# Kernel tuning notes

Hardware: AMD Instinct MI355X
Metric: run time of the kernel (lower is better)

## Reference

```python
import jax, jax.numpy as jnp
import numpy as np
import math

H_IMG, W_IMG = 800, 1216
STRIDES = [4, 8, 16, 32, 64]
SIZES = [32, 64, 128, 256, 512]
RATIOS = [0.5, 1.0, 2.0]
NUM_PER_LEVEL = [(-(-H_IMG // s)) * (-(-W_IMG // s)) * len(RATIOS) for s in STRIDES]
A_TOTAL = sum(NUM_PER_LEVEL)  # 728973
B = 4
PRE_NMS = 1000   # pre_nms_top_n['testing']
POST_NMS = 1000  # post_nms_top_n['testing']
NMS_TH = 0.7
MIN_SIZE = 1e-3
BBOX_XFORM_CLIP = math.log(1000.0 / 16)
NEG = -1e10
LEVELS_NP = np.repeat(np.arange(len(NUM_PER_LEVEL)), NUM_PER_LEVEL).astype(np.int32)


def _make_anchors():
    out = []
    for stride, size in zip(STRIDES, SIZES):
        fh, fw = -(-H_IMG // stride), -(-W_IMG // stride)
        r = np.sqrt(np.asarray(RATIOS, dtype=np.float64))
        ws, hs = size / r, size * r
        base = np.stack([-ws / 2, -hs / 2, ws / 2, hs / 2], axis=1)  # [3,4]
        sx = np.arange(fw, dtype=np.float64) * stride
        sy = np.arange(fh, dtype=np.float64) * stride
        gy, gx = np.meshgrid(sy, sx, indexing='ij')
        shifts = np.stack([gx.ravel(), gy.ravel(), gx.ravel(), gy.ravel()], axis=1)
        out.append((shifts[:, None, :] + base[None]).reshape(-1, 4))
    return np.concatenate(out, 0).astype(np.float32)


def setup_inputs() -> dict:
    key = jax.random.key(0)
    k1, k2 = jax.random.split(key)
    objectness = jax.random.normal(k1, (B, A_TOTAL), dtype=jnp.float32)
    deltas = jax.random.normal(k2, (B, A_TOTAL, 4), dtype=jnp.float32) * 0.2
    anchors = jnp.asarray(_make_anchors())
    return {'objectness': objectness, 'deltas': deltas, 'anchors': anchors}


def _decode(deltas, anchors):
    # BoxCoder.decode with weights (1,1,1,1)
    wa = anchors[:, 2] - anchors[:, 0]
    ha = anchors[:, 3] - anchors[:, 1]
    cxa = anchors[:, 0] + 0.5 * wa
    cya = anchors[:, 1] + 0.5 * ha
    dx, dy = deltas[..., 0], deltas[..., 1]
    dw = jnp.minimum(deltas[..., 2], BBOX_XFORM_CLIP)
    dh = jnp.minimum(deltas[..., 3], BBOX_XFORM_CLIP)
    cx = dx * wa + cxa
    cy = dy * ha + cya
    w = jnp.exp(dw) * wa
    h = jnp.exp(dh) * ha
    return jnp.stack([cx - 0.5 * w, cy - 0.5 * h, cx + 0.5 * w, cy + 0.5 * h], axis=-1)


def _topk_per_level(obj):
    # _get_top_n_idx: independent top-k within each anchor level, indices offset
    idxs, off = [], 0
    for n in NUM_PER_LEVEL:
        k = min(PRE_NMS, n)
        _, ti = jax.lax.top_k(obj[:, off:off + n], k)
        idxs.append(ti + off)
        off += n
    return jnp.concatenate(idxs, axis=1)


def _pairwise_iou(b):
    area = (b[:, 2] - b[:, 0]) * (b[:, 3] - b[:, 1])
    lt = jnp.maximum(b[:, None, :2], b[None, :, :2])
    rb = jnp.minimum(b[:, None, 2:], b[None, :, 2:])
    wh = jnp.clip(rb - lt, 0.0)
    inter = wh[..., 0] * wh[..., 1]
    return inter / (area[:, None] + area[None, :] - inter)


def _filter_image(boxes, scores, lvl):
    # clip_boxes_to_image
    x1 = jnp.clip(boxes[:, 0], 0.0, W_IMG)
    y1 = jnp.clip(boxes[:, 1], 0.0, H_IMG)
    x2 = jnp.clip(boxes[:, 2], 0.0, W_IMG)
    y2 = jnp.clip(boxes[:, 3], 0.0, H_IMG)
    boxes = jnp.stack([x1, y1, x2, y2], axis=1)
    # remove_small_boxes (as a validity mask; fixed shapes under jit)
    valid = ((x2 - x1) >= MIN_SIZE) & ((y2 - y1) >= MIN_SIZE)
    scores = jnp.where(valid, scores, NEG)
    N = boxes.shape[0]
    # batched_nms: offset boxes per level so levels never overlap
    sg_boxes = jax.lax.stop_gradient(boxes)
    offset = lvl.astype(boxes.dtype) * (sg_boxes.max() + 1.0)
    order = jnp.argsort(-jax.lax.stop_gradient(scores))
    iou = _pairwise_iou(sg_boxes[order] + offset[order][:, None])  # [N,N]
    idx = jnp.arange(N)
    def body(i, keep):
        sup = (iou[i] > NMS_TH) & keep[i] & (idx > i)
        return keep & ~sup
    keep = jax.lax.fori_loop(0, N, body, valid[order])
    # kept entries in score order, then truncate to POST_NMS (fixed shape)
    prio = jnp.where(keep, idx, N)
    sel = jnp.argsort(prio)[:POST_NMS]
    kept = keep[sel]
    src = order[sel]
    out_b = jnp.where(kept[:, None], boxes[src], 0.0)
    out_s = jnp.where(kept, scores[src], NEG)
    return out_b, out_s


def reference(objectness, deltas, anchors):
    proposals = _decode(deltas, anchors)                      # [B,A,4]
    top_idx = _topk_per_level(objectness)                     # [B,5000]
    obj_sel = jnp.take_along_axis(objectness, top_idx, axis=1)
    prop_sel = jnp.take_along_axis(proposals, top_idx[..., None], axis=1)
    lvl_sel = jnp.asarray(LEVELS_NP)[top_idx]
    boxes, scores = jax.vmap(_filter_image)(prop_sel, obj_sel, lvl_sel)
    return boxes, scores  # [B,POST_NMS,4], [B,POST_NMS]
```

## Files before the change

### kernel.cpp

```cpp
#include <hip/hip_runtime.h>
#include <stdint.h>

#pragma clang fp contract(off)

#define B_IMGS   4
#define NLVL     5
#define A_TOTAL  242991
#define NSEL     4741
#define NBUCK    8192
#define BSHIFT   19
#define CAND_CAP 2048
#define POST_NMS 1000
#define NBL      (B_IMGS * NLVL)
#define NMS_TH   0.7f
#define NEGV     (-1e10f)
#define W_IMGF   1216.0f
#define H_IMGF   800.0f
#define MIN_SZ   1e-3f
#define BBOX_CLIP 4.135166556742356f

#define NSLICE_PER_IMG 34

__device__ __forceinline__ int lvl_k(int l) { return (l == 4) ? 741 : 1000; }

__device__ __forceinline__ unsigned flipf(float f) {
    unsigned u = __float_as_uint(f);
    return u ^ (unsigned)(((int)u >> 31) | 0x80000000);
}
__device__ __forceinline__ float unflipf(unsigned os) {
    unsigned u = (os & 0x80000000u) ? (os ^ 0x80000000u) : ~os;
    return __uint_as_float(u);
}

__device__ __forceinline__ void async_cp16(const void* g, void* l) {
    __builtin_amdgcn_global_load_lds(
        (const __attribute__((address_space(1))) unsigned*)g,
        (__attribute__((address_space(3))) unsigned*)l,
        16, 0, 0);
}

static constexpr size_t OFF_BM5   = 0;
static constexpr size_t OFF_CNT   = 128;
static constexpr size_t OFF_DI    = 208;
static constexpr size_t OFF_D2    = 224;
static constexpr size_t OFF_HSL   = 256;
static constexpr size_t OFF_PSL   = OFF_HSL  + (size_t)B_IMGS * NSLICE_PER_IMG * NBUCK * 4;
static constexpr size_t OFF_CAND  = OFF_PSL  + (size_t)B_IMGS * NSLICE_PER_IMG * 256 * 4;
static constexpr size_t OFF_SEL   = OFF_CAND + (size_t)NBL * CAND_CAP * 8;
static constexpr size_t OFF_BOXR  = OFF_SEL  + (size_t)B_IMGS * NSEL * 8;
static constexpr size_t OFF_SCR   = OFF_BOXR + (size_t)B_IMGS * NSEL * 16;
static constexpr size_t OFF_BOXL  = OFF_SCR  + (size_t)B_IMGS * NSEL * 4;
static constexpr size_t OFF_VAL   = OFF_BOXL + (size_t)B_IMGS * NSEL * 16;
static constexpr size_t OFF_RMAP  = OFF_VAL  + (size_t)B_IMGS * NSEL * 4;
static constexpr size_t OFF_KEEP  = OFF_RMAP + (size_t)B_IMGS * NSEL * 4;
static constexpr size_t OFF_MASK  = (OFF_KEEP + (size_t)B_IMGS * NSEL * 4 + 15) & ~(size_t)15;
static constexpr size_t WS_NEED   = OFF_MASK + (size_t)NBL * 1024 * 16 * 8;

#define HBLK_PER_IMG 34
__global__ __launch_bounds__(512) void k_hist(const float* __restrict__ obj,
                                              unsigned* __restrict__ hist_sl,
                                              unsigned* __restrict__ part_sl,
                                              unsigned* __restrict__ cntz) {
    __shared__ __align__(16) unsigned lh[NBUCK];
    const int tid = threadIdx.x;
    const int b = blockIdx.x / HBLK_PER_IMG;
    const int r = blockIdx.x - b * HBLK_PER_IMG;
    if (r == 33) {
        if (b == 0 && tid < 28) cntz[tid] = 0;
        return;
    }
    int sofs, sub, chunk, lstart, n;
    if (r < 24)      { sofs = 0;  sub = r;      chunk = 7600; lstart = 0;      n = 182400; }
    else if (r < 30) { sofs = 24; sub = r - 24; chunk = 7600; lstart = 182400; n = 45600; }
    else if (r < 32) { sofs = 30; sub = r - 30; chunk = 5700; lstart = 228000; n = 11400; }
    else             { sofs = 32; sub = 0;      chunk = 2850; lstart = 239400; n = 2850; }
    #pragma unroll
    for (int i = tid; i < NBUCK; i += 512) lh[i] = 0;
    __syncthreads();
    const int s0 = sub * chunk;
    const int m = min(chunk, n - s0);
    const float* src = obj + (size_t)b * A_TOTAL + lstart + s0;
    const int peel0 = (int)(((16u - ((unsigned)(uintptr_t)src & 15u)) & 15u) >> 2);
    const int peel  = (peel0 < m) ? peel0 : m;
    const int nv    = (m - peel) >> 2;
    const float4* s4 = (const float4*)(src + peel);
    const int tail0 = peel + (nv << 2);
#define H1(f) atomicAdd(&lh[flipf(f) >> BSHIFT], 1u)
#define H4(v) do { H1((v).x); H1((v).y); H1((v).z); H1((v).w); } while (0)
    if (tid < peel) H1(src[tid]);
    for (int i = tid; i < nv; i += 2048) {
        if (i + 1536 < nv) {
            float4 a0 = s4[i], a1 = s4[i + 512], a2 = s4[i + 1024], a3 = s4[i + 1536];
            H4(a0); H4(a1); H4(a2); H4(a3);
        } else {
            float4 a0 = s4[i]; H4(a0);
            if (i + 512  < nv) { float4 a = s4[i + 512];  H4(a); }
            if (i + 1024 < nv) { float4 a = s4[i + 1024]; H4(a); }
        }
    }
    for (int i = tail0 + tid; i < m; i += 512) H1(src[i]);
#undef H4
#undef H1
    __syncthreads();
    const int slice = b * NSLICE_PER_IMG + sofs + sub;
    unsigned* gh = hist_sl + (size_t)slice * NBUCK;
    #pragma unroll
    for (int i = tid; i < NBUCK / 4; i += 512)
        ((uint4*)gh)[i] = ((const uint4*)lh)[i];
    if (tid < 256) {
        unsigned s = 0;
        #pragma unroll
        for (int i = 0; i < 32; ++i) s += lh[tid * 32 + ((i + tid) & 31)];
        part_sl[(size_t)slice * 256 + tid] = s;
    }
}

#define CBLK_PER_IMG 65
__global__ __launch_bounds__(256) void k_compact(const float* __restrict__ obj,
                                                 const unsigned* __restrict__ hist_sl,
                                                 const unsigned* __restrict__ part_sl,
                                                 unsigned* __restrict__ cnt,
                                                 unsigned long long* __restrict__ cand) {
    __shared__ unsigned long long sbuf[CAND_CAP];
    __shared__ unsigned wsum[4];
    __shared__ unsigned fcnt[4];
    __shared__ unsigned s_cum, s_thr, lcnt, gbase;
    const int tid = threadIdx.x;
    const int b = blockIdx.x / CBLK_PER_IMG;
    const int r = blockIdx.x - b * CBLK_PER_IMG;
    int l, sofs, nsub, sub, chunk, lstart, n;
    if (r < 48)      { l = 0; sofs = 0;  nsub = 24; sub = r;      chunk = 3800; lstart = 0;      n = 182400; }
    else if (r < 60) { l = 1; sofs = 24; nsub = 6;  sub = r - 48; chunk = 3800; lstart = 182400; n = 45600; }
    else if (r < 63) { l = 2; sofs = 30; nsub = 2;  sub = r - 60; chunk = 3800; lstart = 228000; n = 11400; }
    else if (r == 63){ l = 3; sofs = 32; nsub = 1;  sub = 0;      chunk = 2850; lstart = 239400; n = 2850; }
    else             { l = 4; sofs = 33; nsub = 0;  sub = 0;      chunk = 741;  lstart = 242250; n = 741; }
    const int bl = b * NLVL + l;
    const int kl = lvl_k(l);
    if (tid == 0) { lcnt = 0; s_cum = 0; }
    __syncthreads();
    unsigned T = 0;
    if (l < 4) {
        const int lane = tid & 63, wv = tid >> 6;
        const unsigned* pb = part_sl + (size_t)(b * NSLICE_PER_IMG + sofs) * 256 + (255 - tid);
        unsigned x = 0;
        #pragma unroll 6
        for (int s = 0; s < nsub; ++s) x += pb[(size_t)s * 256];
        #pragma unroll
        for (int d = 1; d < 64; d <<= 1) {
            unsigned up = __shfl_up(x, d);
            if (lane >= d) x += up;
        }
        if (lane == 63) wsum[wv] = x;
        __syncthreads();
        unsigned add = 0;
        #pragma unroll
        for (int u = 0; u < 3; ++u) if (u < wv) add += wsum[u];
        const unsigned suffix = x + add;
        unsigned long long bm = __ballot(suffix >= (unsigned)kl);
        if (lane == 0) fcnt[wv] = (unsigned)__popcll(bm);
        __syncthreads();
        const int chnk = (int)(fcnt[0] + fcnt[1] + fcnt[2] + fcnt[3]) - 1;
        if ((255 - tid) == chnk + 1) s_cum = suffix;
        __syncthreads();
        if (tid < 64) {
            unsigned y = 0;
            if (tid < 32) {
                const unsigned* hb = hist_sl + (size_t)(b * NSLICE_PER_IMG + sofs) * NBUCK
                                   + chnk * 32 + (31 - tid);
                #pragma unroll 6
                for (int s = 0; s < nsub; ++s) y += hb[(size_t)s * NBUCK];
            }
            #pragma unroll
            for (int d = 1; d < 32; d <<= 1) {
                unsigned up = __shfl_up(y, d);
                if (tid >= d) y += up;
            }
            unsigned suf2 = s_cum + y;
            unsigned long long bm2 = __ballot((tid < 32) && (suf2 >= (unsigned)kl));
            if (tid == 0) {
                int istar = (int)__popcll(bm2) - 1;
                s_thr = (unsigned)(chnk * 32 + istar);
            }
        }
        __syncthreads();
        T = s_thr;
    }
    const int s0 = sub * chunk;
    const int m = min(chunk, n - s0);
    const int abase = lstart + s0;
    const float* src = obj + (size_t)b * A_TOTAL + abase;
    const int peel0 = (int)(((16u - ((unsigned)(uintptr_t)src & 15u)) & 15u) >> 2);
    const int peel  = (peel0 < m) ? peel0 : m;
    const int nv    = (m - peel) >> 2;
    const float4* s4 = (const float4*)(src + peel);
    const int tail0 = peel + (nv << 2);
#define E1(f, idx) do { unsigned os_ = flipf(f); \
    if ((os_ >> BSHIFT) >= T) { \
        unsigned slot = atomicAdd(&lcnt, 1u); \
        if (slot < CAND_CAP) \
            sbuf[slot] = (((unsigned long long)(~os_)) << 32) | (unsigned)(idx); \
    } } while (0)
#define E4(v, gb) do { E1((v).x, (gb)); E1((v).y, (gb) + 1); \
                       E1((v).z, (gb) + 2); E1((v).w, (gb) + 3); } while (0)
    if (tid < peel) E1(src[tid], abase + tid);
    for (int i = tid; i < nv; i += 512) {
        const int gb0 = abase + peel + (i << 2);
        if (i + 256 < nv) {
            float4 a0 = s4[i], a1 = s4[i + 256];
            E4(a0, gb0);
            E4(a1, gb0 + 1024);
        } else {
            float4 a0 = s4[i];
            E4(a0, gb0);
        }
    }
    for (int i = tail0 + tid; i < m; i += 256) E1(src[i], abase + i);
#undef E4
#undef E1
    __syncthreads();
    unsigned total = lcnt; if (total > CAND_CAP) total = CAND_CAP;
    if (tid == 0) gbase = atomicAdd(&cnt[bl], total);
    __syncthreads();
    const unsigned gb = gbase;
    for (unsigned i = tid; i < total; i += 256) {
        unsigned g = gb + i;
        if (g < CAND_CAP)
            cand[(size_t)bl * CAND_CAP + g] = sbuf[i];
    }
}

__device__ __forceinline__ int lbound_lds(const unsigned long long* s, int len,
                                          unsigned long long key) {
    int lo = 0, hi = len;
    while (lo < hi) {
        int mid = (lo + hi) >> 1;
        if (s[mid] < key) lo = mid + 1; else hi = mid;
    }
    return lo;
}

__global__ __launch_bounds__(1024) void k_sortdec(
        const unsigned long long* __restrict__ cand, const unsigned* __restrict__ cnt,
        unsigned long long* __restrict__ sel,
        const float* __restrict__ deltas, const float* __restrict__ anchors,
        float* __restrict__ boxes_r, float* __restrict__ score_r,
        float* __restrict__ boxes_l, int* __restrict__ valid_l,
        int* __restrict__ rankmap, unsigned* __restrict__ boxmax5,
        unsigned* __restrict__ bar_i) {
    __shared__ __align__(16) char smem[38016];
    __shared__ float wmax[16];
    const int bl = blockIdx.x;
    const int b = bl / NLVL, l = bl - (bl / NLVL) * NLVL;
    const int tid = threadIdx.x;

    {
        unsigned long long* keys = (unsigned long long*)smem;
        int m = (int)cnt[bl];
        if (m > CAND_CAP) m = CAND_CAP;
        for (int i = tid; i < CAND_CAP; i += 1024)
            keys[i] = (i < m) ? cand[(size_t)bl * CAND_CAP + i] : ~0ULL;
        __syncthreads();
        for (int k = 2; k <= CAND_CAP; k <<= 1) {
            for (int j = k >> 1; j > 0; j >>= 1) {
                int i = ((tid / j) * (j << 1)) + (tid % j);
                int p = i + j;
                bool up = ((i & k) == 0);
                unsigned long long a = keys[i], c = keys[p];
                if ((a > c) == up) { keys[i] = c; keys[p] = a; }
                __syncthreads();
            }
        }
        int kl = lvl_k(l);
        for (int q = tid; q < kl; q += 1024)
            sel[(size_t)b * NSEL + l * 1000 + q] = keys[q];
    }
    __syncthreads();

    if (tid == 0) {
        __threadfence();
        __hip_atomic_fetch_add(bar_i + b, 1u, __ATOMIC_RELAXED, __HIP_MEMORY_SCOPE_AGENT);
        while (__hip_atomic_load(bar_i + b, __ATOMIC_RELAXED, __HIP_MEMORY_SCOPE_AGENT)
               < (unsigned)NLVL)
            __builtin_amdgcn_s_sleep(2);
        __threadfence();
    }
    __syncthreads();

    unsigned long long* skey = (unsigned long long*)smem;
    for (int i = tid; i < NSEL; i += 1024)
        skey[i] = sel[(size_t)b * NSEL + i];
    __syncthreads();
    const int sub = l;
    int p = sub * 1024 + tid;
    bool on = p < NSEL;
    float mx = 0.0f;
    if (on) {
        int l2i = p / 1000;
        int q = p - l2i * 1000;
        unsigned long long key = skey[p];
        unsigned a = (unsigned)(key & 0xFFFFFFFFu);
        unsigned os = ~((unsigned)(key >> 32));
        if (a >= A_TOTAL) a = 0;
        float score = unflipf(os);
        int r = q;
        for (int l2 = 0; l2 < NLVL; ++l2) {
            if (l2 == l2i) continue;
            r += lbound_lds(skey + l2 * 1000, lvl_k(l2), key);
        }
        const float* dv = deltas + ((size_t)b * A_TOTAL + a) * 4;
        const float* av = anchors + (size_t)a * 4;
        float ax1 = av[0], ay1 = av[1], ax2 = av[2], ay2 = av[3];
        float wa = ax2 - ax1, ha = ay2 - ay1;
        float cxa = ax1 + 0.5f * wa, cya = ay1 + 0.5f * ha;
        float dx = dv[0], dy = dv[1];
        float dw = fminf(dv[2], BBOX_CLIP), dh = fminf(dv[3], BBOX_CLIP);
        float cx = dx * wa + cxa, cy = dy * ha + cya;
        float w = expf(dw) * wa, h = expf(dh) * ha;
        float x1 = cx - 0.5f * w, y1 = cy - 0.5f * h;
        float x2 = cx + 0.5f * w, y2 = cy + 0.5f * h;
        float x1c = fminf(fmaxf(x1, 0.0f), W_IMGF);
        float y1c = fminf(fmaxf(y1, 0.0f), H_IMGF);
        float x2c = fminf(fmaxf(x2, 0.0f), W_IMGF);
        float y2c = fminf(fmaxf(y2, 0.0f), H_IMGF);
        int valid = ((x2c - x1c) >= MIN_SZ) && ((y2c - y1c) >= MIN_SZ);
        mx = fmaxf(fmaxf(x1c, y1c), fmaxf(x2c, y2c));
        size_t rp = (size_t)b * NSEL + r;
        boxes_r[rp * 4 + 0] = x1c; boxes_r[rp * 4 + 1] = y1c;
        boxes_r[rp * 4 + 2] = x2c; boxes_r[rp * 4 + 3] = y2c;
        score_r[rp] = score;
        size_t pp = (size_t)b * NSEL + p;
        boxes_l[pp * 4 + 0] = x1c; boxes_l[pp * 4 + 1] = y1c;
        boxes_l[pp * 4 + 2] = x2c; boxes_l[pp * 4 + 3] = y2c;
        valid_l[pp] = valid;
        rankmap[pp] = r;
    }
    #pragma unroll
    for (int o = 32; o > 0; o >>= 1)
        mx = fmaxf(mx, __shfl_xor(mx, o));
    if ((tid & 63) == 0) wmax[tid >> 6] = mx;
    __syncthreads();
    if (tid == 0) {
        float m2 = wmax[0];
        #pragma unroll
        for (int i = 1; i < 16; ++i) m2 = fmaxf(m2, wmax[i]);
        boxmax5[b * 5 + sub] = __float_as_uint(m2);
    }
}

__global__ void k_mask(const float* __restrict__ boxes_l, const unsigned* __restrict__ boxmax5,
                       unsigned long long* __restrict__ mask) {
    int bl = blockIdx.z;
    int b = bl / NLVL, l = bl - b * NLVL;
    int kl = lvl_k(l);
    int w = blockIdx.x, rg = blockIdx.y, tid = threadIdx.x;
    if (rg * 256 >= kl) return;
    float M = __uint_as_float(boxmax5[b * 5 + 0]);
    #pragma unroll
    for (int j = 1; j < 5; ++j) M = fmaxf(M, __uint_as_float(boxmax5[b * 5 + j]));
    M += 1.0f;
    float off = (float)l * M;
    __shared__ float cb[64][5];
    int j0 = w * 64;
    if (tid < 64) {
        int j = j0 + tid;
        if (j < kl) {
            const float* bp = boxes_l + ((size_t)b * NSEL + l * 1000 + j) * 4;
            float x1 = bp[0] + off, y1 = bp[1] + off, x2 = bp[2] + off, y2 = bp[3] + off;
            cb[tid][0] = x1; cb[tid][1] = y1; cb[tid][2] = x2; cb[tid][3] = y2;
            cb[tid][4] = (x2 - x1) * (y2 - y1);
        }
    }
    __syncthreads();
    int i = rg * 256 + tid;
    if (i >= kl) return;
    unsigned long long word = 0;
    if (j0 + 63 > i) {
        const float* bp = boxes_l + ((size_t)b * NSEL + l * 1000 + i) * 4;
        float ix1 = bp[0] + off, iy1 = bp[1] + off, ix2 = bp[2] + off, iy2 = bp[3] + off;
        float ai = (ix2 - ix1) * (iy2 - iy1);
        int jmax = min(64, kl - j0);
        for (int bb = 0; bb < jmax; ++bb) {
            int jj = j0 + bb;
            if (jj <= i) continue;
            float ltx = fmaxf(ix1, cb[bb][0]), lty = fmaxf(iy1, cb[bb][1]);
            float rbx = fminf(ix2, cb[bb][2]), rby = fminf(iy2, cb[bb][3]);
            float ww = fmaxf(rbx - ltx, 0.0f), hh = fmaxf(rby - lty, 0.0f);
            float inter = ww * hh;
            float iou = inter / ((ai + cb[bb][4]) - inter);
            if (iou > NMS_TH) word |= (1ULL << bb);
        }
    }
    mask[((size_t)bl * 1024 + i) * 16 + w] = word;
}

__global__ __launch_bounds__(256) void k_resout(const int* __restrict__ valid_l,
                                                const int* __restrict__ rankmap,
                                                const unsigned long long* __restrict__ mask,
                                                int* __restrict__ keep_r,
                                                unsigned* __restrict__ done2,
                                                const float* __restrict__ boxes_r,
                                                const float* __restrict__ score_r,
                                                float* __restrict__ out) {
    __shared__ __align__(16) unsigned long long sb[16 * 1024];
    __shared__ int ps[256];
    __shared__ int s_flag;
    const int bl = blockIdx.x;
    const int b = bl / NLVL, l = bl - b * NLVL;
    const int kl = lvl_k(l);
    const int tid = threadIdx.x;
    const int lane = tid & 63;
    const int base = b * NSEL + l * 1000;
    const int nch = (kl + 63) >> 6;
    const char* mbyte = (const char*)(mask + (size_t)bl * 1024 * 16);

    unsigned long long keep_w = 0;
    if (tid < 64) {
        for (int c = 0; c < nch; ++c) {
            const char* g = mbyte + (size_t)c * 8192 + (size_t)lane * 16;
            char* d = (char*)sb + (size_t)c * 8192;
            #pragma unroll
            for (int j = 0; j < 8; ++j)
                async_cp16(g + j * 1024, d + j * 1024);
        }
        for (int c = 0; c < 16; ++c) {
            int q = c * 64 + lane;
            int vv = (q < kl) ? valid_l[base + q] : 0;
            unsigned long long bm = __ballot(vv);
            if (lane == c) keep_w = bm;
        }
    }
    __syncthreads();

    if (tid < 64) {
        for (int c = 0; c < nch; ++c) {
            unsigned long long* cur = sb + (size_t)c * 1024;
            unsigned long long kw = __shfl(keep_w, c);
            if (kw) {
                unsigned long long diag = cur[lane * 16 + c];
                unsigned dlo = (unsigned)diag, dhi = (unsigned)(diag >> 32);
                unsigned long long nz = __ballot(diag != 0ULL);
                unsigned long long rem = kw & nz;
                while (rem) {
                    int rr = __ffsll((long long)rem) - 1;
                    unsigned lo = __builtin_amdgcn_readlane(dlo, rr);
                    unsigned hi = __builtin_amdgcn_readlane(dhi, rr);
                    unsigned long long d = ((unsigned long long)hi << 32) | lo;
                    kw &= ~d;
                    rem &= ~(d | (1ULL << rr));
                }
                unsigned long long supp = 0;
                if (lane < 16) {
                    #pragma unroll
                    for (int rr = 0; rr < 64; ++rr) {
                        unsigned long long mm = cur[rr * 16 + lane];
                        supp |= (((kw >> rr) & 1ULL) ? mm : 0ULL);
                    }
                }
                if (lane == c) keep_w = kw;
                else if (lane < 16 && lane > c) keep_w &= ~supp;
            }
        }
        for (int c = 0; c < 16; ++c) {
            unsigned long long kwc = __shfl(keep_w, c);
            int q = c * 64 + lane;
            if (q < kl)
                keep_r[b * NSEL + rankmap[base + q]] = (int)((kwc >> lane) & 1ULL);
        }
    }
    __syncthreads();

    if (tid == 0) {
        __threadfence();
        unsigned old = __hip_atomic_fetch_add(done2 + b, 1u,
                                              __ATOMIC_ACQ_REL, __HIP_MEMORY_SCOPE_AGENT);
        s_flag = (old == NLVL - 1);
        if (old == NLVL - 1) __threadfence();
    }
    __syncthreads();
    if (!s_flag) return;

    float* ob = out + (size_t)b * POST_NMS * 4;
    float* osc = out + (size_t)B_IMGS * POST_NMS * 4 + (size_t)b * POST_NMS;
    for (int p = tid; p < POST_NMS; p += 256) {
        ob[p * 4 + 0] = 0.0f; ob[p * 4 + 1] = 0.0f;
        ob[p * 4 + 2] = 0.0f; ob[p * 4 + 3] = 0.0f;
        osc[p] = NEGV;
    }
    __syncthreads();
    const int CH = 19;
    int basei = tid * CH;
    int c0 = 0;
    #pragma unroll
    for (int k = 0; k < CH; ++k) {
        int rr = basei + k;
        if (rr < NSEL) c0 += keep_r[b * NSEL + rr];
    }
    ps[tid] = c0;
    __syncthreads();
    for (int ofs = 1; ofs < 256; ofs <<= 1) {
        int v = (tid >= ofs) ? ps[tid - ofs] : 0;
        __syncthreads();
        ps[tid] += v;
        __syncthreads();
    }
    int p = ps[tid] - c0;
    #pragma unroll
    for (int k = 0; k < CH; ++k) {
        int rr = basei + k;
        if (rr < NSEL && keep_r[b * NSEL + rr]) {
            if (p < POST_NMS) {
                const float* bp = boxes_r + ((size_t)b * NSEL + rr) * 4;
                ob[p * 4 + 0] = bp[0]; ob[p * 4 + 1] = bp[1];
                ob[p * 4 + 2] = bp[2]; ob[p * 4 + 3] = bp[3];
                osc[p] = score_r[(size_t)b * NSEL + rr];
            }
            ++p;
        }
    }
}

extern "C" void kernel_launch(void* const* d_in, const int* in_sizes, int n_in,
                              void* d_out, int out_size, void* d_ws, size_t ws_size,
                              hipStream_t stream) {
    const float* obj     = (const float*)d_in[0];
    const float* deltas  = (const float*)d_in[1];
    const float* anchors = (const float*)d_in[2];
    float* out = (float*)d_out;

    char* ws = (char*)d_ws;
    unsigned*            boxmax5 = (unsigned*)(ws + OFF_BM5);
    unsigned*            cnt     = (unsigned*)(ws + OFF_CNT);
    unsigned*            bar_i   = (unsigned*)(ws + OFF_DI);
    unsigned*            done2   = (unsigned*)(ws + OFF_D2);
    unsigned*            hist_sl = (unsigned*)(ws + OFF_HSL);
    unsigned*            part_sl = (unsigned*)(ws + OFF_PSL);
    unsigned long long*  cand    = (unsigned long long*)(ws + OFF_CAND);
    unsigned long long*  sel     = (unsigned long long*)(ws + OFF_SEL);
    float*               boxes_r = (float*)(ws + OFF_BOXR);
    float*               score_r = (float*)(ws + OFF_SCR);
    float*               boxes_l = (float*)(ws + OFF_BOXL);
    int*                 valid_l = (int*)(ws + OFF_VAL);
    int*                 rankmap = (int*)(ws + OFF_RMAP);
    int*                 keep_r  = (int*)(ws + OFF_KEEP);
    unsigned long long*  maskp   = (unsigned long long*)(ws + OFF_MASK);

    (void)in_sizes; (void)n_in; (void)out_size; (void)ws_size; (void)WS_NEED;

    k_hist<<<B_IMGS * HBLK_PER_IMG, 512, 0, stream>>>(obj, hist_sl, part_sl, cnt);
    k_compact<<<B_IMGS * CBLK_PER_IMG, 256, 0, stream>>>(obj, hist_sl, part_sl, cnt, cand);
    k_sortdec<<<NBL, 1024, 0, stream>>>(cand, cnt, sel, deltas, anchors,
                                        boxes_r, score_r, boxes_l, valid_l,
                                        rankmap, boxmax5, bar_i);
    k_mask<<<dim3(16, 4, NBL), 256, 0, stream>>>(boxes_l, boxmax5, maskp);
    k_resout<<<NBL, 256, 0, stream>>>(valid_l, rankmap, maskp, keep_r, done2,
                                      boxes_r, score_r, out);
}
```

Before: 179.4 us.

## Replace bitmask NMS with sparse edge list and parallel fixed-point suppression

Instead of writing a dense 64-bit IoU mask per box pair and resolving it with a serial single-wave scan, the mask kernel appends each overlapping (victim, suppressor) pair to a per-level edge list through atomics. The resolve kernel loads the edges into shared memory and iterates a parallel Jacobi-style relaxation until the keep vector stops changing. This cuts mask memory traffic and the serial dependency chain when edges are sparse. The trade-off is global atomic contention, a hard edge cap that silently drops overflowing edges, and a number of iterations that depends on suppression-chain depth, each iteration paying several block barriers.

Result: slower. 238.3 us (+32.8%).

```diff
diff --git a/kernel.cpp b/kernel.cpp
--- a/kernel.cpp
+++ b/kernel.cpp
@@ -20,6 +20,7 @@
 #define BBOX_CLIP 4.135166556742356f
 
 #define NSLICE_PER_IMG 34
+#define ECAP     8192
 
 __device__ __forceinline__ int lvl_k(int l) { return (l == 4) ? 741 : 1000; }
 
@@ -30,20 +31,14 @@
 __device__ __forceinline__ float unflipf(unsigned os) {
     unsigned u = (os & 0x80000000u) ? (os ^ 0x80000000u) : ~os;
     return __uint_as_float(u);
-}
-
-__device__ __forceinline__ void async_cp16(const void* g, void* l) {
-    __builtin_amdgcn_global_load_lds(
-        (const __attribute__((address_space(1))) unsigned*)g,
-        (__attribute__((address_space(3))) unsigned*)l,
-        16, 0, 0);
 }
 
 static constexpr size_t OFF_BM5   = 0;
 static constexpr size_t OFF_CNT   = 128;
 static constexpr size_t OFF_DI    = 208;
 static constexpr size_t OFF_D2    = 224;
-static constexpr size_t OFF_HSL   = 256;
+static constexpr size_t OFF_ECNT  = 240;
+static constexpr size_t OFF_HSL   = 320;
 static constexpr size_t OFF_PSL   = OFF_HSL  + (size_t)B_IMGS * NSLICE_PER_IMG * NBUCK * 4;
 static constexpr size_t OFF_CAND  = OFF_PSL  + (size_t)B_IMGS * NSLICE_PER_IMG * 256 * 4;
 static constexpr size_t OFF_SEL   = OFF_CAND + (size_t)NBL * CAND_CAP * 8;
@@ -53,8 +48,8 @@
 static constexpr size_t OFF_VAL   = OFF_BOXL + (size_t)B_IMGS * NSEL * 16;
 static constexpr size_t OFF_RMAP  = OFF_VAL  + (size_t)B_IMGS * NSEL * 4;
 static constexpr size_t OFF_KEEP  = OFF_RMAP + (size_t)B_IMGS * NSEL * 4;
-static constexpr size_t OFF_MASK  = (OFF_KEEP + (size_t)B_IMGS * NSEL * 4 + 15) & ~(size_t)15;
-static constexpr size_t WS_NEED   = OFF_MASK + (size_t)NBL * 1024 * 16 * 8;
+static constexpr size_t OFF_EDGE  = (OFF_KEEP + (size_t)B_IMGS * NSEL * 4 + 15) & ~(size_t)15;
+static constexpr size_t WS_NEED   = OFF_EDGE + (size_t)NBL * ECAP * 4;
 
 #define HBLK_PER_IMG 34
 __global__ __launch_bounds__(512) void k_hist(const float* __restrict__ obj,
@@ -66,7 +61,7 @@
     const int b = blockIdx.x / HBLK_PER_IMG;
     const int r = blockIdx.x - b * HBLK_PER_IMG;
     if (r == 33) {
-        if (b == 0 && tid < 28) cntz[tid] = 0;
+        if (b == 0 && tid < 48) cntz[tid] = 0;
         return;
     }
     int sofs, sub, chunk, lstart, n;
@@ -347,8 +342,8 @@
     }
 }
 
-__global__ void k_mask(const float* __restrict__ boxes_l, const unsigned* __restrict__ boxmax5,
-                       unsigned long long* __restrict__ mask) {
+__global__ void k_edges(const float* __restrict__ boxes_l, const unsigned* __restrict__ boxmax5,
+                        unsigned* __restrict__ ecnt, unsigned* __restrict__ edges) {
     int bl = blockIdx.z;
     int b = bl / NLVL, l = bl - b * NLVL;
     int kl = lvl_k(l);
@@ -373,7 +368,6 @@
     __syncthreads();
     int i = rg * 256 + tid;
     if (i >= kl) return;
-    unsigned long long word = 0;
     if (j0 + 63 > i) {
         const float* bp = boxes_l + ((size_t)b * NSEL + l * 1000 + i) * 4;
         float ix1 = bp[0] + off, iy1 = bp[1] + off, ix2 = bp[2] + off, iy2 = bp[3] + off;
@@ -387,86 +381,68 @@
             float ww = fmaxf(rbx - ltx, 0.0f), hh = fmaxf(rby - lty, 0.0f);
             float inter = ww * hh;
             float iou = inter / ((ai + cb[bb][4]) - inter);
-            if (iou > NMS_TH) word |= (1ULL << bb);
-        }
-    }
-    mask[((size_t)bl * 1024 + i) * 16 + w] = word;
+            if (iou > NMS_TH) {
+                unsigned slot = atomicAdd(&ecnt[bl], 1u);
+                if (slot < ECAP)
+                    edges[(size_t)bl * ECAP + slot] = ((unsigned)jj << 16) | (unsigned)i;
+            }
+        }
+    }
 }
 
 __global__ __launch_bounds__(256) void k_resout(const int* __restrict__ valid_l,
                                                 const int* __restrict__ rankmap,
-                                                const unsigned long long* __restrict__ mask,
+                                                const unsigned* __restrict__ ecnt,
+                                                const unsigned* __restrict__ edges,
                                                 int* __restrict__ keep_r,
                                                 unsigned* __restrict__ done2,
                                                 const float* __restrict__ boxes_r,
                                                 const float* __restrict__ score_r,
                                                 float* __restrict__ out) {
-    __shared__ __align__(16) unsigned long long sb[16 * 1024];
+    __shared__ unsigned se[ECAP];
+    __shared__ int ka[1000], kb[1000], sval[1000];
     __shared__ int ps[256];
-    __shared__ int s_flag;
+    __shared__ int s_chg, s_flag;
     const int bl = blockIdx.x;
     const int b = bl / NLVL, l = bl - b * NLVL;
     const int kl = lvl_k(l);
     const int tid = threadIdx.x;
-    const int lane = tid & 63;
     const int base = b * NSEL + l * 1000;
-    const int nch = (kl + 63) >> 6;
-    const char* mbyte = (const char*)(mask + (size_t)bl * 1024 * 16);
-
-    unsigned long long keep_w = 0;
-    if (tid < 64) {
-        for (int c = 0; c < nch; ++c) {
-            const char* g = mbyte + (size_t)c * 8192 + (size_t)lane * 16;
-            char* d = (char*)sb + (size_t)c * 8192;
-            #pragma unroll
-            for (int j = 0; j < 8; ++j)
-                async_cp16(g + j * 1024, d + j * 1024);
-        }
-        for (int c = 0; c < 16; ++c) {
-            int q = c * 64 + lane;
-            int vv = (q < kl) ? valid_l[base + q] : 0;
-            unsigned long long bm = __ballot(vv);
-            if (lane == c) keep_w = bm;
-        }
-    }
-    __syncthreads();
-
-    if (tid < 64) {
-        for (int c = 0; c < nch; ++c) {
-            unsigned long long* cur = sb + (size_t)c * 1024;
-            unsigned long long kw = __shfl(keep_w, c);
-            if (kw) {
-                unsigned long long diag = cur[lane * 16 + c];
-                unsigned dlo = (unsigned)diag, dhi = (unsigned)(diag >> 32);
-                unsigned long long nz = __ballot(diag != 0ULL);
-                unsigned long long rem = kw & nz;
-                while (rem) {
-                    int rr = __ffsll((long long)rem) - 1;
-                    unsigned lo = __builtin_amdgcn_readlane(dlo, rr);
-                    unsigned hi = __builtin_amdgcn_readlane(dhi, rr);
-                    unsigned long long d = ((unsigned long long)hi << 32) | lo;
-                    kw &= ~d;
-                    rem &= ~(d | (1ULL << rr));
-                }
-                unsigned long long supp = 0;
-                if (lane < 16) {
-                    #pragma unroll
-                    for (int rr = 0; rr < 64; ++rr) {
-                        unsigned long long mm = cur[rr * 16 + lane];
-                        supp |= (((kw >> rr) & 1ULL) ? mm : 0ULL);
-                    }
-                }
-                if (lane == c) keep_w = kw;
-                else if (lane < 16 && lane > c) keep_w &= ~supp;
-            }
-        }
-        for (int c = 0; c < 16; ++c) {
-            unsigned long long kwc = __shfl(keep_w, c);
-            int q = c * 64 + lane;
-            if (q < kl)
-                keep_r[b * NSEL + rankmap[base + q]] = (int)((kwc >> lane) & 1ULL);
-        }
-    }
+
+    int E = (int)ecnt[bl];
+    if (E > ECAP) E = ECAP;
+    for (int i = tid; i < E; i += 256)
+        se[i] = edges[(size_t)bl * ECAP + i];
+    for (int q = tid; q < kl; q += 256) {
+        int v = valid_l[base + q];
+        sval[q] = v;
+        ka[q] = v;
+    }
+    __syncthreads();
+
+    int* cur = ka;
+    int* nxt = kb;
+    for (int it = 0; it < kl; ++it) {
+        for (int q = tid; q < kl; q += 256) nxt[q] = sval[q];
+        if (tid == 0) s_chg = 0;
+        __syncthreads();
+        for (int e = tid; e < E; e += 256) {
+            unsigned pe = se[e];
+            int vi = (int)(pe >> 16), sj = (int)(pe & 0xFFFFu);
+            if (cur[sj]) nxt[vi] = 0;
+        }
+        __syncthreads();
+        int chg = 0;
+        for (int q = tid; q < kl; q += 256) if (nxt[q] != cur[q]) chg = 1;
+        if (chg) s_chg = 1;
+        __syncthreads();
+        int stop = (s_chg == 0);
+        __syncthreads();
+        int* t = cur; cur = nxt; nxt = t;
+        if (stop) break;
+    }
+    for (int q = tid; q < kl; q += 256)
+        keep_r[b * NSEL + rankmap[base + q]] = cur[q];
     __syncthreads();
 
     if (tid == 0) {
@@ -532,6 +508,7 @@
     unsigned*            cnt     = (unsigned*)(ws + OFF_CNT);
     unsigned*            bar_i   = (unsigned*)(ws + OFF_DI);
     unsigned*            done2   = (unsigned*)(ws + OFF_D2);
+    unsigned*            ecnt    = (unsigned*)(ws + OFF_ECNT);
     unsigned*            hist_sl = (unsigned*)(ws + OFF_HSL);
     unsigned*            part_sl = (unsigned*)(ws + OFF_PSL);
     unsigned long long*  cand    = (unsigned long long*)(ws + OFF_CAND);
@@ -542,7 +519,7 @@
     int*                 valid_l = (int*)(ws + OFF_VAL);
     int*                 rankmap = (int*)(ws + OFF_RMAP);
     int*                 keep_r  = (int*)(ws + OFF_KEEP);
-    unsigned long long*  maskp   = (unsigned long long*)(ws + OFF_MASK);
+    unsigned*            edgesp  = (unsigned*)(ws + OFF_EDGE);
 
     (void)in_sizes; (void)n_in; (void)out_size; (void)ws_size; (void)WS_NEED;
 
@@ -551,7 +528,7 @@
     k_sortdec<<<NBL, 1024, 0, stream>>>(cand, cnt, sel, deltas, anchors,
                                         boxes_r, score_r, boxes_l, valid_l,
                                         rankmap, boxmax5, bar_i);
-    k_mask<<<dim3(16, 4, NBL), 256, 0, stream>>>(boxes_l, boxmax5, maskp);
-    k_resout<<<NBL, 256, 0, stream>>>(valid_l, rankmap, maskp, keep_r, done2,
+    k_edges<<<dim3(16, 4, NBL), 256, 0, stream>>>(boxes_l, boxmax5, ecnt, edgesp);
+    k_resout<<<NBL, 256, 0, stream>>>(valid_l, rankmap, ecnt, edgesp, keep_r, done2,
                                       boxes_r, score_r, out);
 }
```
